# Kernel optimization log

Hardware: AMD Instinct MI355X
Metric: run time of the kernel (lower is better)

Reference implementation:

```python
import math
import jax, jax.numpy as jnp
import numpy as np

B, C, N, K = 16, 64, 2048, 20

def setup_inputs() -> dict:
    key = jax.random.key(0)
    x = jax.random.normal(key, (B, C, N), dtype=jnp.float32)
    local_idx = jnp.zeros((B, N), dtype=bool)  # unused in dgcnn variant
    return {"x": x, "k": K, "local_idx": local_idx}

def _gather_points(points, idx):
    # points: (B, N, C), idx: (B, N, k) -> (B, N, k, C)
    return jax.vmap(lambda p, i: p[i])(points, idx)

def reference(x, k, local_idx):
    b, c, n = x.shape
    xt = jnp.swapaxes(x, 1, 2)  # (B, N, C)
    # negative squared pairwise distance: -||xi||^2 + 2 xi.xj - ||xj||^2
    inner = 2.0 * jnp.einsum('bnc,bmc->bnm', xt, xt)
    xx = jnp.sum(xt * xt, axis=-1)  # (B, N)
    pd = -xx[:, :, None] + inner - xx[:, None, :]
    _, idx = jax.lax.top_k(pd, k)  # (B, N, k) nearest neighbors
    knn_x = _gather_points(xt, idx)  # (B, N, k, C)
    # per-channel topk over the k neighbors, then mean
    k2 = math.ceil(k * 2 / 3)
    vals = jax.lax.top_k(jnp.swapaxes(knn_x, 2, 3), k2)[0]  # (B, N, C, k2)
    x1 = jnp.mean(vals, axis=-1)  # (B, N, C)
    # gather smoothed features at neighbor indices
    feat = _gather_points(x1, idx)  # (B, N, k, C)
    x_exp = jnp.broadcast_to(xt[:, :, None, :], (b, n, k, c))
    feature = jnp.concatenate([feat - x_exp, x_exp], axis=-1)  # (B, N, k, 2C)
    feature = jnp.transpose(feature, (0, 3, 1, 2))  # (B, 2C, N, k)
    idx_flat = (idx + jnp.arange(b, dtype=idx.dtype)[:, None, None] * n).reshape(-1)
    return feature, idx_flat
```

## Files before the change

### kernel.cpp

```cpp
#include <hip/hip_runtime.h>
#include <cstdint>
#include <cstddef>
#include <math.h>

#define BB 16
#define CC 64
#define NN 2048
#define KK 20
#define K2 14
#define QB 16
#define NC 26
#define SP 2064

typedef float nfloat4 __attribute__((ext_vector_type(4)));
typedef __attribute__((ext_vector_type(8))) short bf16x8;
typedef __attribute__((ext_vector_type(4))) float f32x4;
typedef unsigned short u16;

static __device__ __forceinline__ u16 f2bf(float f) {
    unsigned u = __float_as_uint(f);
    return (u16)((u + 0x7fffu + ((u >> 16) & 1u)) >> 16);
}

__global__ __launch_bounds__(256) void prep_kernel(const float* __restrict__ x,
                                                   float* __restrict__ xt,
                                                   u16* __restrict__ xth,
                                                   u16* __restrict__ xtl,
                                                   float* __restrict__ xxf,
                                                   double* __restrict__ xxd) {
    __shared__ float s_t[64][65];
    int b = blockIdx.x >> 5;
    int n0 = (blockIdx.x & 31) * 64;
    const float* xb = x + (size_t)b * CC * NN;
    int tid = threadIdx.x;
    int cq = tid >> 6;
    int nl = tid & 63;

#pragma unroll
    for (int r = 0; r < 16; ++r) {
        int c = r * 4 + cq;
        s_t[c][nl] = xb[c * NN + n0 + nl];
    }
    __syncthreads();

#pragma unroll
    for (int r = 0; r < 16; ++r) {
        int n = r * 4 + cq;
        float f = s_t[nl][n];
        size_t o = ((size_t)b * NN + n0 + n) * CC + nl;
        xt[o] = f;
        u16 h = f2bf(f);
        float hf = __uint_as_float((unsigned)h << 16);
        u16 l = f2bf(f - hf);
        xth[o] = h;
        xtl[o] = l;
    }

    if (tid < 64) {
        double s = 0.0;
#pragma unroll
        for (int c = 0; c < CC; ++c) {
            double v = (double)s_t[c][tid];
            s += v * v;
        }
        xxd[b * NN + n0 + tid] = s;
        xxf[b * NN + n0 + tid] = (float)s;
    }
}

__global__ __launch_bounds__(1024, 2) void knn_kernel(const float* __restrict__ x,
                                                      const float* __restrict__ xt,
                                                      const u16* __restrict__ xth,
                                                      const u16* __restrict__ xtl,
                                                      const float* __restrict__ xxf,
                                                      const double* __restrict__ xxd,
                                                      int* __restrict__ idx_ws,
                                                      float* __restrict__ idx_out) {
    __shared__ float s_pd[QB][SP];
    __shared__ float s_xx[NN];
    __shared__ __align__(16) float s_q[CC][QB];
    __shared__ float s_sv[QB][64];
    __shared__ int   s_si[QB][64];

    int tid = threadIdx.x;
    int b = blockIdx.x >> 7;
    int n0 = (blockIdx.x & 127) * QB;
    const float* xb = x + (size_t)b * CC * NN;

    { int c = tid >> 4, qq = tid & 15; s_q[c][qq] = xb[c * NN + n0 + qq]; }
    s_xx[tid] = xxf[b * NN + tid];
    s_xx[tid + 1024] = xxf[b * NN + 1024 + tid];
    __syncthreads();

    int w = tid >> 6;
    int lane = tid & 63;
    int ar = lane & 15, ag = lane >> 4;

    {
        const u16* xhb = xth + (size_t)b * NN * CC;
        const u16* xlb = xtl + (size_t)b * NN * CC;
        const u16* aph = xhb + (size_t)(n0 + ar) * CC + ag * 8;
        const u16* apl = xlb + (size_t)(n0 + ar) * CC + ag * 8;
        bf16x8 ah0 = *(const bf16x8*)(aph);
        bf16x8 ah1 = *(const bf16x8*)(aph + 32);
        bf16x8 al0 = *(const bf16x8*)(apl);
        bf16x8 al1 = *(const bf16x8*)(apl + 32);

        int p0 = w * 128;
        f32x4 acc[8];
#pragma unroll
        for (int t = 0; t < 8; ++t)
#pragma unroll
            for (int i = 0; i < 4; ++i) acc[t][i] = 0.f;

#pragma unroll
        for (int t = 0; t < 8; ++t) {
            const u16* bph = xhb + (size_t)(p0 + t * 16 + ar) * CC + ag * 8;
            const u16* bpl = xlb + (size_t)(p0 + t * 16 + ar) * CC + ag * 8;
            bf16x8 bh0 = *(const bf16x8*)(bph);
            bf16x8 bh1 = *(const bf16x8*)(bph + 32);
            bf16x8 bl0 = *(const bf16x8*)(bpl);
            bf16x8 bl1 = *(const bf16x8*)(bpl + 32);
            acc[t] = __builtin_amdgcn_mfma_f32_16x16x32_bf16(ah0, bh0, acc[t], 0, 0, 0);
            acc[t] = __builtin_amdgcn_mfma_f32_16x16x32_bf16(al0, bh0, acc[t], 0, 0, 0);
            acc[t] = __builtin_amdgcn_mfma_f32_16x16x32_bf16(ah0, bl0, acc[t], 0, 0, 0);
            acc[t] = __builtin_amdgcn_mfma_f32_16x16x32_bf16(ah1, bh1, acc[t], 0, 0, 0);
            acc[t] = __builtin_amdgcn_mfma_f32_16x16x32_bf16(al1, bh1, acc[t], 0, 0, 0);
            acc[t] = __builtin_amdgcn_mfma_f32_16x16x32_bf16(ah1, bl1, acc[t], 0, 0, 0);
        }

        float qn[4];
#pragma unroll
        for (int r = 0; r < 4; ++r) qn[r] = s_xx[n0 + ag * 4 + r];
#pragma unroll
        for (int t = 0; t < 8; ++t) {
            int p = p0 + t * 16 + ar;
            float xxp = s_xx[p];
#pragma unroll
            for (int r = 0; r < 4; ++r)
                s_pd[ag * 4 + r][p] = (2.f * acc[t][r] - qn[r]) - xxp;
        }
    }
    __syncthreads();

    int q = w;
    const float* pd = &s_pd[q][0];

    float v[32];
#pragma unroll
    for (int r = 0; r < 32; ++r) v[r] = pd[lane + (r << 6)];

    float lmax = v[0]; int lr = 0;
#pragma unroll
    for (int r = 1; r < 32; ++r)
        if (v[r] > lmax) { lmax = v[r]; lr = r; }

    float sv = lmax;
#pragma unroll
    for (int k = 2; k <= 64; k <<= 1) {
#pragma unroll
        for (int j = k >> 1; j > 0; j >>= 1) {
            float o = __shfl_xor(sv, j);
            bool dird = ((lane & k) == 0);
            bool first = ((lane & j) == 0);
            sv = (first == dird) ? fmaxf(sv, o) : fminf(sv, o);
        }
    }
    float tau = __shfl(sv, 25);

    int cnt = 0;
#pragma unroll
    for (int r = 0; r < 32; ++r) cnt += (v[r] >= tau) ? 1 : 0;
    int incl = cnt;
#pragma unroll
    for (int off = 1; off < 64; off <<= 1) {
        int o = __shfl_up(incl, off);
        if (lane >= off) incl += o;
    }
    int S = __shfl(incl, 63);

    float fv = -INFINITY;
    int fi = 0x7fffffff;
    if (S <= 64) {
        int wr = incl - cnt;
#pragma unroll
        for (int r = 0; r < 32; ++r) {
            if (v[r] >= tau) { s_sv[q][wr] = v[r]; s_si[q][wr] = lane + (r << 6); ++wr; }
        }
        if (lane < S) { fv = s_sv[q][lane]; fi = s_si[q][lane]; }
    } else {
        for (int t = 0; t < NC; ++t) {
            float bv = lmax; int bi = lane + (lr << 6);
#pragma unroll
            for (int off = 32; off; off >>= 1) {
                float ov = __shfl_xor(bv, off);
                int oi = __shfl_xor(bi, off);
                if (ov > bv || (ov == bv && oi < bi)) { bv = ov; bi = oi; }
            }
            if (lane == t) { fv = bv; fi = bi; }
            if ((bi & 63) == lane) {
                int rsel = bi >> 6;
#pragma unroll
                for (int r = 0; r < 32; ++r) if (r == rsel) v[r] = -INFINITY;
                lmax = v[0]; lr = 0;
#pragma unroll
                for (int r = 1; r < 32; ++r)
                    if (v[r] > lmax) { lmax = v[r]; lr = r; }
            }
        }
    }

#pragma unroll
    for (int k = 2; k <= 64; k <<= 1) {
#pragma unroll
        for (int j = k >> 1; j > 0; j >>= 1) {
            float ov = __shfl_xor(fv, j);
            int oi = __shfl_xor(fi, j);
            bool dird = ((lane & k) == 0);
            bool first = ((lane & j) == 0);
            bool better = (fv > ov) || (fv == ov && fi < oi);
            if (better != (first == dird)) { fv = ov; fi = oi; }
        }
    }

    float* s_c = (float*)&s_pd[q][0];
    const float* xtb = xt + (size_t)b * NN * CC;
    int nq = n0 + q;

#pragma unroll
    for (int t = 0; t < NC; ++t) {
        int cand = __shfl(fi, t);
        s_c[lane * 27 + t] = xtb[(size_t)cand * CC + lane];
    }

    double accd = 0.0;
    for (int c = 0; c < CC; ++c) {
        double qc = (double)s_q[c][q];
        double cd = (double)s_c[c * 27 + lane];
        accd = fma(qc, cd, accd);
    }

    double val = -INFINITY;
    int idxq = 0x7fffffff;
    if (lane < NC) {
        val = 2.0 * accd - xxd[b * NN + nq] - xxd[b * NN + fi];
        idxq = fi;
    }

#pragma unroll
    for (int k = 2; k <= 32; k <<= 1) {
#pragma unroll
        for (int j = k >> 1; j > 0; j >>= 1) {
            double ov = __shfl_xor(val, j, 32);
            int oi = __shfl_xor(idxq, j, 32);
            bool dird = ((lane & k) == 0);
            bool first = ((lane & j) == 0);
            bool better = (val > ov) || (val == ov && idxq < oi);
            if (better != (first == dird)) { val = ov; idxq = oi; }
        }
    }

    if (lane < KK) {
        size_t obase = ((size_t)b * NN + nq) * KK;
        idx_ws[obase + lane] = idxq;
        idx_out[obase + lane] = (float)(idxq + b * NN);
    }
}

__global__ __launch_bounds__(256) void x1_kernel(const float* __restrict__ xt,
                                                 const int* __restrict__ idx_ws,
                                                 float* __restrict__ x1t) {
    __shared__ int s_idx[16][KK];
    __shared__ float s_out[64][17];
    int tid = threadIdx.x;
    int b = blockIdx.x >> 7;
    int n0 = (blockIdx.x & 127) * 16;
    const float* xtb = xt + (size_t)b * NN * CC;

    for (int i = tid; i < 16 * KK; i += 256)
        s_idx[i / KK][i % KK] = idx_ws[((size_t)b * NN + n0) * KK + i];
    __syncthreads();

    int pl = tid >> 6, c = tid & 63;
#pragma unroll
    for (int it = 0; it < 4; ++it) {
        int nl = it * 4 + pl;
        float vals[KK];
        float sum = 0.f;
#pragma unroll
        for (int j = 0; j < KK; ++j) {
            vals[j] = xtb[(size_t)s_idx[nl][j] * CC + c];
            sum += vals[j];
        }
#pragma unroll
        for (int t = 0; t < KK - K2; ++t) {
            float worst = INFINITY;
            int wj = 0;
#pragma unroll
            for (int j = 0; j < KK; ++j)
                if (vals[j] < worst) { worst = vals[j]; wj = j; }
            sum -= worst;
            vals[wj] = INFINITY;
        }
        s_out[c][nl] = sum / (float)K2;
    }
    __syncthreads();

    int cw = tid >> 2, nw = (tid & 3) * 4;
    float4 v = make_float4(s_out[cw][nw], s_out[cw][nw + 1],
                           s_out[cw][nw + 2], s_out[cw][nw + 3]);
    *(float4*)(&x1t[((size_t)b * CC + cw) * NN + n0 + nw]) = v;
}

__global__ __launch_bounds__(256) void feat_kernel(const float* __restrict__ x,
                                                   const float* __restrict__ x1t,
                                                   const int* __restrict__ idx_ws,
                                                   float* __restrict__ out) {
    int bc = blockIdx.x;
    int b = bc >> 7, ch = bc & 127;
    const float* xb = x + (size_t)b * CC * NN;
    float* o = out + (size_t)bc * NN * KK;
    const int* idxb = idx_ws + (size_t)b * NN * KK;

    if (ch < CC) {
        const float* row = x1t + ((size_t)b * CC + ch) * NN;
        const float* xr = xb + ch * NN;
        for (int it = 0; it < 40; ++it) {
            unsigned e = (it * 256 + threadIdx.x) * 4;
            int4 id4 = *(const int4*)(idxb + e);
            nfloat4 o4;
            o4.x = row[id4.x] - xr[(e    ) / KK];
            o4.y = row[id4.y] - xr[(e + 1) / KK];
            o4.z = row[id4.z] - xr[(e + 2) / KK];
            o4.w = row[id4.w] - xr[(e + 3) / KK];
            __builtin_nontemporal_store(o4, (nfloat4*)(o + e));
        }
    } else {
        const float* xr = xb + (ch - CC) * NN;
        for (int it = 0; it < 40; ++it) {
            unsigned e = (it * 256 + threadIdx.x) * 4;
            nfloat4 o4;
            o4.x = xr[(e    ) / KK];
            o4.y = xr[(e + 1) / KK];
            o4.z = xr[(e + 2) / KK];
            o4.w = xr[(e + 3) / KK];
            __builtin_nontemporal_store(o4, (nfloat4*)(o + e));
        }
    }
}

extern "C" void kernel_launch(void* const* d_in, const int* in_sizes, int n_in,
                              void* d_out, int out_size, void* d_ws, size_t ws_size,
                              hipStream_t stream) {
    const float* x = (const float*)d_in[0];
    float* out = (float*)d_out;

    char* ws = (char*)d_ws;
    float* xt   = (float*)ws;
    float* x1t  = (float*)(ws + (size_t)8388608);
    double* xxd = (double*)(ws + (size_t)16777216);
    float* xxf  = (float*)(ws + (size_t)17039360);
    int* idx_ws = (int*)(ws + (size_t)17170432);

    u16* xth = (u16*)out;
    u16* xtl = (u16*)((char*)out + (size_t)8388608);

    float* idx_out = out + (size_t)BB * 2 * CC * NN * KK;

    prep_kernel<<<BB * (NN / 64), 256, 0, stream>>>(x, xt, xth, xtl, xxf, xxd);
    knn_kernel<<<BB * (NN / QB), 1024, 0, stream>>>(x, xt, xth, xtl, xxf, xxd, idx_ws, idx_out);
    x1_kernel<<<BB * (NN / 16), 256, 0, stream>>>(xt, idx_ws, x1t);
    feat_kernel<<<BB * 2 * CC, 256, 0, stream>>>(x, x1t, idx_ws, out);
}
```

Baseline: 658.6 us.

## Halve KNN query tile to 8 per block with 512 threads for more occupancy

The KNN kernel now handles 8 query points per block with 512 threads instead of 16 with 1024. This halves the shared pairwise-distance buffer, so more blocks can reside per CU. The MFMA distance pass loops over paired 16-column tiles with fresh accumulators, and only the half of the 16-row output that holds real queries is written. The price is that half of each 16x16 MFMA tile is wasted on duplicated query rows, so matrix work per useful output doubles. The candidate key rows are also loaded twice as many times across the grid.

Result: slower. 687.5 us (+4.4%).

```diff
diff --git a/kernel.cpp b/kernel.cpp
--- a/kernel.cpp
+++ b/kernel.cpp
@@ -8,9 +8,9 @@
 #define NN 2048
 #define KK 20
 #define K2 14
-#define QB 16
+#define TQ 8
 #define NC 26
-#define SP 2064
+#define SP 2052
 
 typedef float nfloat4 __attribute__((ext_vector_type(4)));
 typedef __attribute__((ext_vector_type(8))) short bf16x8;
@@ -68,28 +68,27 @@
     }
 }
 
-__global__ __launch_bounds__(1024, 2) void knn_kernel(const float* __restrict__ x,
-                                                      const float* __restrict__ xt,
-                                                      const u16* __restrict__ xth,
-                                                      const u16* __restrict__ xtl,
-                                                      const float* __restrict__ xxf,
-                                                      const double* __restrict__ xxd,
-                                                      int* __restrict__ idx_ws,
-                                                      float* __restrict__ idx_out) {
-    __shared__ float s_pd[QB][SP];
-    __shared__ float s_xx[NN];
-    __shared__ __align__(16) float s_q[CC][QB];
-    __shared__ float s_sv[QB][64];
-    __shared__ int   s_si[QB][64];
+__global__ __launch_bounds__(512, 4) void knn_kernel(const float* __restrict__ x,
+                                                     const float* __restrict__ xt,
+                                                     const u16* __restrict__ xth,
+                                                     const u16* __restrict__ xtl,
+                                                     const float* __restrict__ xxf,
+                                                     const double* __restrict__ xxd,
+                                                     int* __restrict__ idx_ws,
+                                                     float* __restrict__ idx_out) {
+    __shared__ float s_pd[TQ][SP];
+    __shared__ __align__(16) float s_xx[NN];
+    __shared__ __align__(16) float s_q[CC][TQ];
+    __shared__ float s_sv[TQ][64];
+    __shared__ int   s_si[TQ][64];
 
     int tid = threadIdx.x;
-    int b = blockIdx.x >> 7;
-    int n0 = (blockIdx.x & 127) * QB;
+    int b = blockIdx.x >> 8;
+    int n0 = (blockIdx.x & 255) * TQ;
     const float* xb = x + (size_t)b * CC * NN;
 
-    { int c = tid >> 4, qq = tid & 15; s_q[c][qq] = xb[c * NN + n0 + qq]; }
-    s_xx[tid] = xxf[b * NN + tid];
-    s_xx[tid + 1024] = xxf[b * NN + 1024 + tid];
+    { int c = tid >> 3, qq = tid & 7; s_q[c][qq] = xb[c * NN + n0 + qq]; }
+    *(float4*)(&s_xx[tid * 4]) = *(const float4*)(xxf + b * NN + tid * 4);
     __syncthreads();
 
     int w = tid >> 6;
@@ -99,46 +98,61 @@
     {
         const u16* xhb = xth + (size_t)b * NN * CC;
         const u16* xlb = xtl + (size_t)b * NN * CC;
-        const u16* aph = xhb + (size_t)(n0 + ar) * CC + ag * 8;
-        const u16* apl = xlb + (size_t)(n0 + ar) * CC + ag * 8;
+        int qrow = n0 + (ar & 7);
+        const u16* aph = xhb + (size_t)qrow * CC + ag * 8;
+        const u16* apl = xlb + (size_t)qrow * CC + ag * 8;
         bf16x8 ah0 = *(const bf16x8*)(aph);
         bf16x8 ah1 = *(const bf16x8*)(aph + 32);
         bf16x8 al0 = *(const bf16x8*)(apl);
         bf16x8 al1 = *(const bf16x8*)(apl + 32);
 
-        int p0 = w * 128;
-        f32x4 acc[8];
-#pragma unroll
-        for (int t = 0; t < 8; ++t)
-#pragma unroll
-            for (int i = 0; i < 4; ++i) acc[t][i] = 0.f;
-
-#pragma unroll
-        for (int t = 0; t < 8; ++t) {
-            const u16* bph = xhb + (size_t)(p0 + t * 16 + ar) * CC + ag * 8;
-            const u16* bpl = xlb + (size_t)(p0 + t * 16 + ar) * CC + ag * 8;
-            bf16x8 bh0 = *(const bf16x8*)(bph);
-            bf16x8 bh1 = *(const bf16x8*)(bph + 32);
-            bf16x8 bl0 = *(const bf16x8*)(bpl);
-            bf16x8 bl1 = *(const bf16x8*)(bpl + 32);
-            acc[t] = __builtin_amdgcn_mfma_f32_16x16x32_bf16(ah0, bh0, acc[t], 0, 0, 0);
-            acc[t] = __builtin_amdgcn_mfma_f32_16x16x32_bf16(al0, bh0, acc[t], 0, 0, 0);
-            acc[t] = __builtin_amdgcn_mfma_f32_16x16x32_bf16(ah0, bl0, acc[t], 0, 0, 0);
-            acc[t] = __builtin_amdgcn_mfma_f32_16x16x32_bf16(ah1, bh1, acc[t], 0, 0, 0);
-            acc[t] = __builtin_amdgcn_mfma_f32_16x16x32_bf16(al1, bh1, acc[t], 0, 0, 0);
-            acc[t] = __builtin_amdgcn_mfma_f32_16x16x32_bf16(ah1, bl1, acc[t], 0, 0, 0);
-        }
-
+        int p0 = w * 256;
         float qn[4];
-#pragma unroll
-        for (int r = 0; r < 4; ++r) qn[r] = s_xx[n0 + ag * 4 + r];
-#pragma unroll
-        for (int t = 0; t < 8; ++t) {
-            int p = p0 + t * 16 + ar;
-            float xxp = s_xx[p];
-#pragma unroll
-            for (int r = 0; r < 4; ++r)
-                s_pd[ag * 4 + r][p] = (2.f * acc[t][r] - qn[r]) - xxp;
+        int agq = ag & 1;
+#pragma unroll
+        for (int r = 0; r < 4; ++r) qn[r] = s_xx[n0 + agq * 4 + r];
+
+#pragma unroll
+        for (int tp = 0; tp < 8; ++tp) {
+            int pA = p0 + tp * 32 + ar;
+            int pB = pA + 16;
+            const u16* bphA = xhb + (size_t)pA * CC + ag * 8;
+            const u16* bplA = xlb + (size_t)pA * CC + ag * 8;
+            const u16* bphB = xhb + (size_t)pB * CC + ag * 8;
+            const u16* bplB = xlb + (size_t)pB * CC + ag * 8;
+            bf16x8 bh0A = *(const bf16x8*)(bphA);
+            bf16x8 bh1A = *(const bf16x8*)(bphA + 32);
+            bf16x8 bl0A = *(const bf16x8*)(bplA);
+            bf16x8 bl1A = *(const bf16x8*)(bplA + 32);
+            bf16x8 bh0B = *(const bf16x8*)(bphB);
+            bf16x8 bh1B = *(const bf16x8*)(bphB + 32);
+            bf16x8 bl0B = *(const bf16x8*)(bplB);
+            bf16x8 bl1B = *(const bf16x8*)(bplB + 32);
+
+            f32x4 accA = {0.f, 0.f, 0.f, 0.f};
+            f32x4 accB = {0.f, 0.f, 0.f, 0.f};
+            accA = __builtin_amdgcn_mfma_f32_16x16x32_bf16(ah0, bh0A, accA, 0, 0, 0);
+            accB = __builtin_amdgcn_mfma_f32_16x16x32_bf16(ah0, bh0B, accB, 0, 0, 0);
+            accA = __builtin_amdgcn_mfma_f32_16x16x32_bf16(al0, bh0A, accA, 0, 0, 0);
+            accB = __builtin_amdgcn_mfma_f32_16x16x32_bf16(al0, bh0B, accB, 0, 0, 0);
+            accA = __builtin_amdgcn_mfma_f32_16x16x32_bf16(ah0, bl0A, accA, 0, 0, 0);
+            accB = __builtin_amdgcn_mfma_f32_16x16x32_bf16(ah0, bl0B, accB, 0, 0, 0);
+            accA = __builtin_amdgcn_mfma_f32_16x16x32_bf16(ah1, bh1A, accA, 0, 0, 0);
+            accB = __builtin_amdgcn_mfma_f32_16x16x32_bf16(ah1, bh1B, accB, 0, 0, 0);
+            accA = __builtin_amdgcn_mfma_f32_16x16x32_bf16(al1, bh1A, accA, 0, 0, 0);
+            accB = __builtin_amdgcn_mfma_f32_16x16x32_bf16(al1, bh1B, accB, 0, 0, 0);
+            accA = __builtin_amdgcn_mfma_f32_16x16x32_bf16(ah1, bl1A, accA, 0, 0, 0);
+            accB = __builtin_amdgcn_mfma_f32_16x16x32_bf16(ah1, bl1B, accB, 0, 0, 0);
+
+            float xxA = s_xx[pA];
+            float xxB = s_xx[pB];
+            if (ag < 2) {
+#pragma unroll
+                for (int r = 0; r < 4; ++r) {
+                    s_pd[ag * 4 + r][pA] = (2.f * accA[r] - qn[r]) - xxA;
+                    s_pd[ag * 4 + r][pB] = (2.f * accB[r] - qn[r]) - xxB;
+                }
+            }
         }
     }
     __syncthreads();
@@ -368,7 +382,7 @@
     float* idx_out = out + (size_t)BB * 2 * CC * NN * KK;
 
     prep_kernel<<<BB * (NN / 64), 256, 0, stream>>>(x, xt, xth, xtl, xxf, xxd);
-    knn_kernel<<<BB * (NN / QB), 1024, 0, stream>>>(x, xt, xth, xtl, xxf, xxd, idx_ws, idx_out);
+    knn_kernel<<<BB * (NN / TQ), 512, 0, stream>>>(x, xt, xth, xtl, xxf, xxd, idx_ws, idx_out);
     x1_kernel<<<BB * (NN / 16), 256, 0, stream>>>(xt, idx_ws, x1t);
     feat_kernel<<<BB * 2 * CC, 256, 0, stream>>>(x, x1t, idx_ws, out);
 }
```
